# Kernel optimization log

Measured on AMD Instinct MI355X. Metric: run time of the kernel, lower is better.

## Reference

```python
import jax, jax.numpy as jnp
import numpy as np

HSIZE = 128
E = 640000


def _init_linear(key, fan_in, fan_out):
    # torch nn.Linear default init: U(-1/sqrt(fan_in), 1/sqrt(fan_in))
    kw, kb = jax.random.split(key)
    bound = 1.0 / np.sqrt(fan_in)
    W = jax.random.uniform(kw, (fan_in, fan_out), jnp.float32, -bound, bound)
    b = jax.random.uniform(kb, (fan_out,), jnp.float32, -bound, bound)
    return W, b


def setup_inputs() -> dict:
    key = jax.random.key(0)
    ks = jax.random.split(key, 6)
    hself = jax.random.normal(ks[0], (E, HSIZE), jnp.float32)
    hother = jax.random.normal(ks[1], (E, HSIZE), jnp.float32)
    Wm1, bm1 = _init_linear(ks[2], 2 * HSIZE, HSIZE)
    Wm2, bm2 = _init_linear(ks[3], HSIZE, HSIZE)
    Wu1, bu1 = _init_linear(ks[4], 2 * HSIZE, HSIZE)
    Wu2, bu2 = _init_linear(ks[5], HSIZE, HSIZE)
    return {"hself": hself, "hother": hother,
            "Wm1": Wm1, "bm1": bm1, "Wm2": Wm2, "bm2": bm2,
            "Wu1": Wu1, "bu1": bu1, "Wu2": Wu2, "bu2": bu2}


def _mlp2(a, b, W1, b1, W2, b2):
    # concat([a, b], -1) @ W1 done without materializing the concat
    h = a @ W1[:HSIZE] + b @ W1[HSIZE:] + b1
    h = jax.nn.relu(h)
    return h @ W2 + b2


def reference(hself, hother, Wm1, bm1, Wm2, bm2, Wu1, bu1, Wu2, bu2):
    # msg: Linear(2h,h) -> ReLU -> Linear(h,h) on cat([hself, hother])
    msg = _mlp2(hself, hother, Wm1, bm1, Wm2, bm2)
    # upd: Linear(2h,h) -> ReLU -> Linear(h,h) on cat([hself, msg])
    out = _mlp2(hself, msg, Wu1, bu1, Wu2, bu2)
    return out
```

## Files before the change

### kernel.cpp

```cpp
#include <hip/hip_runtime.h>

typedef __bf16 bf16_t;
typedef __bf16 bf16x8 __attribute__((ext_vector_type(8)));
typedef float f32x4 __attribute__((ext_vector_type(4)));

#define MFMA(a, b, c) __builtin_amdgcn_mfma_f32_16x16x32_bf16((a), (b), (c), 0, 0, 0)

#define E_ROWS 640000
#define BM 256
#define NTILE 2500
#define GRID 250

static __device__ __forceinline__ bf16x8 cvt8(float4 a, float4 b) {
  bf16x8 r;
  r[0] = (bf16_t)a.x; r[1] = (bf16_t)a.y; r[2] = (bf16_t)a.z; r[3] = (bf16_t)a.w;
  r[4] = (bf16_t)b.x; r[5] = (bf16_t)b.y; r[6] = (bf16_t)b.z; r[7] = (bf16_t)b.w;
  return r;
}

static __device__ __forceinline__ unsigned int pk2(float a, float b) {
  unsigned short ua = __builtin_bit_cast(unsigned short, (bf16_t)a);
  unsigned short ub = __builtin_bit_cast(unsigned short, (bf16_t)b);
  return ((unsigned int)ub << 16) | ua;
}

static __device__ __forceinline__ void gload_lds16(const void* g, void* l) {
  __builtin_amdgcn_global_load_lds(
      (const __attribute__((address_space(1))) unsigned int*)g,
      (__attribute__((address_space(3))) unsigned int*)l, 16, 0, 0);
}

__global__ __launch_bounds__(256) void prep_weights(
    const float* __restrict__ Wm1, const float* __restrict__ Wm2,
    const float* __restrict__ Wu1, const float* __restrict__ Wu2,
    bf16_t* __restrict__ wt) {
  int c = blockIdx.x * 256 + threadIdx.x;
  if (c >= 12288) return;
  int lane = c & 63, f = c >> 6;
  const float* W; int base;
  if (f < 64)       { W = Wm1; base = 0;   }
  else if (f < 96)  { W = Wm2; base = 64;  }
  else if (f < 160) { W = Wu1; base = 96;  }
  else              { W = Wu2; base = 160; }
  int fl = f - base;
  int ks = fl >> 3, nb = fl & 7;
  int k0 = 32 * ks + 8 * (lane >> 4);
  int n  = 16 * nb + (lane & 15);
  bf16x8 v;
  #pragma unroll
  for (int j = 0; j < 8; ++j) v[j] = (bf16_t)W[(size_t)(k0 + j) * 128 + n];
  ((bf16x8*)wt)[c] = v;
}

#define STAGE96(tc0) { \
  _Pragma("unroll") \
  for (int i_ = 0; i_ < 12; ++i_) \
    gload_lds16((const char*)wt + ((size_t)((tc0) + i_ * 512 + tid)) * 16, \
                smem + (i_ * 512 + tid) * 16); }

#define LDW8(s, base, fl0) \
  s##0 = *(const bf16x8*)((base) + ((fl0) + 0) * 1024 + lane * 16); \
  s##1 = *(const bf16x8*)((base) + ((fl0) + 1) * 1024 + lane * 16); \
  s##2 = *(const bf16x8*)((base) + ((fl0) + 2) * 1024 + lane * 16); \
  s##3 = *(const bf16x8*)((base) + ((fl0) + 3) * 1024 + lane * 16); \
  s##4 = *(const bf16x8*)((base) + ((fl0) + 4) * 1024 + lane * 16); \
  s##5 = *(const bf16x8*)((base) + ((fl0) + 5) * 1024 + lane * 16); \
  s##6 = *(const bf16x8*)((base) + ((fl0) + 6) * 1024 + lane * 16); \
  s##7 = *(const bf16x8*)((base) + ((fl0) + 7) * 1024 + lane * 16);

#define ROUND(s, x0, x1) \
  acc00 = MFMA(s##0, x0, acc00); acc10 = MFMA(s##0, x1, acc10); \
  acc01 = MFMA(s##1, x0, acc01); acc11 = MFMA(s##1, x1, acc11); \
  acc02 = MFMA(s##2, x0, acc02); acc12 = MFMA(s##2, x1, acc12); \
  acc03 = MFMA(s##3, x0, acc03); acc13 = MFMA(s##3, x1, acc13); \
  acc04 = MFMA(s##4, x0, acc04); acc14 = MFMA(s##4, x1, acc14); \
  acc05 = MFMA(s##5, x0, acc05); acc15 = MFMA(s##5, x1, acc15); \
  acc06 = MFMA(s##6, x0, acc06); acc16 = MFMA(s##6, x1, acc16); \
  acc07 = MFMA(s##7, x0, acc07); acc17 = MFMA(s##7, x1, acc17);

#define ACCINIT(bp) { const float* bp_ = (bp) + g * 4; float4 q; \
  q = *(const float4*)(bp_ +   0); acc00 = (f32x4){q.x,q.y,q.z,q.w}; acc10 = acc00; \
  q = *(const float4*)(bp_ +  16); acc01 = (f32x4){q.x,q.y,q.z,q.w}; acc11 = acc01; \
  q = *(const float4*)(bp_ +  32); acc02 = (f32x4){q.x,q.y,q.z,q.w}; acc12 = acc02; \
  q = *(const float4*)(bp_ +  48); acc03 = (f32x4){q.x,q.y,q.z,q.w}; acc13 = acc03; \
  q = *(const float4*)(bp_ +  64); acc04 = (f32x4){q.x,q.y,q.z,q.w}; acc14 = acc04; \
  q = *(const float4*)(bp_ +  80); acc05 = (f32x4){q.x,q.y,q.z,q.w}; acc15 = acc05; \
  q = *(const float4*)(bp_ +  96); acc06 = (f32x4){q.x,q.y,q.z,q.w}; acc16 = acc06; \
  q = *(const float4*)(bp_ + 112); acc07 = (f32x4){q.x,q.y,q.z,q.w}; acc17 = acc07; }

#define RPK_H(av, nb, R) { \
  f32x4 v = av; \
  float e0 = v[0], e1 = v[1], e2 = v[2], e3 = v[3]; \
  if (R) { e0 = fmaxf(e0, 0.f); e1 = fmaxf(e1, 0.f); \
           e2 = fmaxf(e2, 0.f); e3 = fmaxf(e3, 0.f); } \
  uint2 w; w.x = pk2(e0, e1); w.y = pk2(e2, e3); \
  int dl = c + 16 * (2 * ((nb) & 1) + (g >> 1)); \
  *(uint2*)(myrep + (((nb) >> 1) * 64 + dl) * 16 + (g & 1) * 8) = w; }

#define WAITLDS asm volatile("s_waitcnt lgkmcnt(0)" ::: "memory");
#define VMCNT0  asm volatile("s_waitcnt vmcnt(0)" ::: "memory");
#define VMCNT16 asm volatile("s_waitcnt vmcnt(16)" ::: "memory");

#define REPACK(R, x) \
  RPK_H(acc00, 0, R) RPK_H(acc01, 1, R) RPK_H(acc02, 2, R) RPK_H(acc03, 3, R) \
  RPK_H(acc04, 4, R) RPK_H(acc05, 5, R) RPK_H(acc06, 6, R) RPK_H(acc07, 7, R) \
  WAITLDS \
  x##00 = *(const bf16x8*)(myrep + (0 * 64 + lane) * 16); \
  x##01 = *(const bf16x8*)(myrep + (1 * 64 + lane) * 16); \
  x##02 = *(const bf16x8*)(myrep + (2 * 64 + lane) * 16); \
  x##03 = *(const bf16x8*)(myrep + (3 * 64 + lane) * 16); \
  WAITLDS \
  RPK_H(acc10, 0, R) RPK_H(acc11, 1, R) RPK_H(acc12, 2, R) RPK_H(acc13, 3, R) \
  RPK_H(acc14, 4, R) RPK_H(acc15, 5, R) RPK_H(acc16, 6, R) RPK_H(acc17, 7, R) \
  WAITLDS \
  x##10 = *(const bf16x8*)(myrep + (0 * 64 + lane) * 16); \
  x##11 = *(const bf16x8*)(myrep + (1 * 64 + lane) * 16); \
  x##12 = *(const bf16x8*)(myrep + (2 * 64 + lane) * 16); \
  x##13 = *(const bf16x8*)(myrep + (3 * 64 + lane) * 16); \
  WAITLDS

#define LOADX(d0, d1, basep, kk, rr0, rr1) { \
  float4 a0 = *(const float4*)((basep) + (rr0) + (kk) * 32); \
  float4 a1 = *(const float4*)((basep) + (rr0) + (kk) * 32 + 4); \
  float4 b0 = *(const float4*)((basep) + (rr1) + (kk) * 32); \
  float4 b1 = *(const float4*)((basep) + (rr1) + (kk) * 32 + 4); \
  d0 = cvt8(a0, a1); d1 = cvt8(b0, b1); }

#define LOADX4(pfx, basep, rr0, rr1) \
  LOADX(pfx##00, pfx##10, basep, 0, rr0, rr1) \
  LOADX(pfx##01, pfx##11, basep, 1, rr0, rr1) \
  LOADX(pfx##02, pfx##12, basep, 2, rr0, rr1) \
  LOADX(pfx##03, pfx##13, basep, 3, rr0, rr1)

#define ST(av, mt, nb, rb) { f32x4 v = av; \
  *(float4*)(out + ((rb) + (mt) * 16 + c) * 128 + (nb) * 16 + g * 4) = \
      (float4){v[0], v[1], v[2], v[3]}; }

#define FIRST_HALF(hs, x) \
  ACCINIT(bm1) \
  LDW8(wa, W1, 0)   ROUND(wa, hs##00, hs##10) \
  LDW8(wa, W1, 8)   ROUND(wa, hs##01, hs##11) \
  LDW8(wa, W1, 16)  ROUND(wa, hs##02, hs##12) \
  LDW8(wa, W1, 24)  ROUND(wa, hs##03, hs##13) \
  LDW8(wa, W1, 32)  ROUND(wa, x##00, x##10) \
  LDW8(wa, W1, 40)  ROUND(wa, x##01, x##11) \
  LDW8(wa, W1, 48)  ROUND(wa, x##02, x##12) \
  LDW8(wa, W1, 56)  ROUND(wa, x##03, x##13) \
  REPACK(true, x) \
  ACCINIT(bm2) \
  LDW8(wa, W2, 0)   ROUND(wa, x##00, x##10) \
  LDW8(wa, W2, 8)   ROUND(wa, x##01, x##11) \
  LDW8(wa, W2, 16)  ROUND(wa, x##02, x##12) \
  LDW8(wa, W2, 24)  ROUND(wa, x##03, x##13) \
  REPACK(false, x)

#define SECOND_HALF(hs, x, rb) \
  ACCINIT(bu1) \
  LDW8(wa, W1, 0)   ROUND(wa, hs##00, hs##10) \
  LDW8(wa, W1, 8)   ROUND(wa, hs##01, hs##11) \
  LDW8(wa, W1, 16)  ROUND(wa, hs##02, hs##12) \
  LDW8(wa, W1, 24)  ROUND(wa, hs##03, hs##13) \
  LDW8(wa, W1, 32)  ROUND(wa, x##00, x##10) \
  LDW8(wa, W1, 40)  ROUND(wa, x##01, x##11) \
  LDW8(wa, W1, 48)  ROUND(wa, x##02, x##12) \
  LDW8(wa, W1, 56)  ROUND(wa, x##03, x##13) \
  REPACK(true, x) \
  ACCINIT(bu2) \
  LDW8(wa, W2, 0)   ROUND(wa, x##00, x##10) \
  LDW8(wa, W2, 8)   ROUND(wa, x##01, x##11) \
  LDW8(wa, W2, 16)  ROUND(wa, x##02, x##12) \
  LDW8(wa, W2, 24)  ROUND(wa, x##03, x##13) \
  ST(acc00, 0, 0, rb) ST(acc01, 0, 1, rb) ST(acc02, 0, 2, rb) ST(acc03, 0, 3, rb) \
  ST(acc04, 0, 4, rb) ST(acc05, 0, 5, rb) ST(acc06, 0, 6, rb) ST(acc07, 0, 7, rb) \
  ST(acc10, 1, 0, rb) ST(acc11, 1, 1, rb) ST(acc12, 1, 2, rb) ST(acc13, 1, 3, rb) \
  ST(acc14, 1, 4, rb) ST(acc15, 1, 5, rb) ST(acc16, 1, 6, rb) ST(acc17, 1, 7, rb)

__global__ __launch_bounds__(512) void fused_mp(
    const float* __restrict__ hself, const float* __restrict__ hother,
    const bf16_t* __restrict__ wt,
    const float* __restrict__ bm1, const float* __restrict__ bm2,
    const float* __restrict__ bu1, const float* __restrict__ bu2,
    float* __restrict__ out) {
  __shared__ char smem[131072];

  const int tid = threadIdx.x;
  const int lane = tid & 63;
  const int wave = tid >> 6;
  const int c = lane & 15;
  const int g = lane >> 4;

  char* W1 = smem;
  char* W2 = smem + 65536;
  char* myrep = smem + 98304 + wave * 4096;

  bf16x8 hsA00, hsA01, hsA02, hsA03, hsA10, hsA11, hsA12, hsA13;
  bf16x8 xA00, xA01, xA02, xA03, xA10, xA11, xA12, xA13;
  bf16x8 hsB00, hsB01, hsB02, hsB03, hsB10, hsB11, hsB12, hsB13;
  bf16x8 xB00, xB01, xB02, xB03, xB10, xB11, xB12, xB13;
  f32x4 acc00, acc01, acc02, acc03, acc04, acc05, acc06, acc07;
  f32x4 acc10, acc11, acc12, acc13, acc14, acc15, acc16, acc17;
  bf16x8 wa0, wa1, wa2, wa3, wa4, wa5, wa6, wa7;

  {
    STAGE96(0)
    __builtin_amdgcn_sched_barrier(0);
    size_t rb = (size_t)blockIdx.x * BM + wave * 32;
    size_t rr0 = (rb + c) * 128 + g * 8, rr1 = rr0 + 2048;
    LOADX4(hsA, hself, rr0, rr1)
    LOADX4(xA, hother, rr0, rr1)
    VMCNT0
    __syncthreads();
  }

  #pragma unroll 1
  for (int it = 0; it < 5; ++it) {
    const int tA = blockIdx.x + it * 500;
    const int tB = tA + 250;
    int tN = tA + 500; if (tN >= NTILE) tN = 0;

    const size_t rbA = (size_t)tA * BM + wave * 32;
    const size_t rbB = (size_t)tB * BM + wave * 32;
    const size_t rbN = (size_t)tN * BM + wave * 32;
    const size_t r0B = (rbB + c) * 128 + g * 8, r1B = r0B + 2048;
    const size_t r0N = (rbN + c) * 128 + g * 8, r1N = r0N + 2048;

    FIRST_HALF(hsA, xA)
    __syncthreads();
    STAGE96(6144)
    __builtin_amdgcn_sched_barrier(0);
    LOADX4(xB, hother, r0B, r1B)
    VMCNT16
    __syncthreads();
    SECOND_HALF(hsA, xA, rbA)
    __syncthreads();
    LOADX4(hsB, hself, r0B, r1B)
    STAGE96(0)
    VMCNT0
    __syncthreads();

    FIRST_HALF(hsB, xB)
    __syncthreads();
    STAGE96(6144)
    __builtin_amdgcn_sched_barrier(0);
    LOADX4(xA, hother, r0N, r1N)
    VMCNT16
    __syncthreads();
    SECOND_HALF(hsB, xB, rbB)
    __syncthreads();
    LOADX4(hsA, hself, r0N, r1N)
    STAGE96(0)
    VMCNT0
    __syncthreads();
  }
}

extern "C" void kernel_launch(void* const* d_in, const int* in_sizes, int n_in,
                              void* d_out, int out_size, void* d_ws, size_t ws_size,
                              hipStream_t stream) {
  const float* hself  = (const float*)d_in[0];
  const float* hother = (const float*)d_in[1];
  const float* Wm1 = (const float*)d_in[2];
  const float* bm1 = (const float*)d_in[3];
  const float* Wm2 = (const float*)d_in[4];
  const float* bm2 = (const float*)d_in[5];
  const float* Wu1 = (const float*)d_in[6];
  const float* bu1 = (const float*)d_in[7];
  const float* Wu2 = (const float*)d_in[8];
  const float* bu2 = (const float*)d_in[9];
  float* out = (float*)d_out;
  bf16_t* wt = (bf16_t*)d_ws;

  prep_weights<<<48, 256, 0, stream>>>(Wm1, Wm2, Wu1, Wu2, wt);
  fused_mp<<<GRID, 512, 0, stream>>>(hself, hother, wt,
                                     bm1, bm2, bu1, bu2, out);
}
```

Baseline: 345.0 us.

## Reschedule hself loads and output stores to overlap with weight staging

Drops the double-buffered hself registers: hself for each tile is now loaded right before its first MLP instead of being prefetched. Output stores move after the weight restaging, separated by scheduling barriers, so the stores overlap with the LDS staging. The last iteration no longer prefetches a dummy tile. This frees registers and removes redundant loads, but exposes the hself load latency at the start of each tile.

After: 340.9 us. No clear change (-1.2%).

```diff
diff --git a/kernel.cpp b/kernel.cpp
--- a/kernel.cpp
+++ b/kernel.cpp
@@ -100,6 +100,7 @@
 #define WAITLDS asm volatile("s_waitcnt lgkmcnt(0)" ::: "memory");
 #define VMCNT0  asm volatile("s_waitcnt vmcnt(0)" ::: "memory");
 #define VMCNT16 asm volatile("s_waitcnt vmcnt(16)" ::: "memory");
+#define SBAR    __builtin_amdgcn_sched_barrier(0);
 
 #define REPACK(R, x) \
   RPK_H(acc00, 0, R) RPK_H(acc01, 1, R) RPK_H(acc02, 2, R) RPK_H(acc03, 3, R) \
@@ -136,12 +137,18 @@
   *(float4*)(out + ((rb) + (mt) * 16 + c) * 128 + (nb) * 16 + g * 4) = \
       (float4){v[0], v[1], v[2], v[3]}; }
 
-#define FIRST_HALF(hs, x) \
+#define STORE16(rb) \
+  ST(acc00, 0, 0, rb) ST(acc01, 0, 1, rb) ST(acc02, 0, 2, rb) ST(acc03, 0, 3, rb) \
+  ST(acc04, 0, 4, rb) ST(acc05, 0, 5, rb) ST(acc06, 0, 6, rb) ST(acc07, 0, 7, rb) \
+  ST(acc10, 1, 0, rb) ST(acc11, 1, 1, rb) ST(acc12, 1, 2, rb) ST(acc13, 1, 3, rb) \
+  ST(acc14, 1, 4, rb) ST(acc15, 1, 5, rb) ST(acc16, 1, 6, rb) ST(acc17, 1, 7, rb)
+
+#define FIRST_HALF(x) \
   ACCINIT(bm1) \
-  LDW8(wa, W1, 0)   ROUND(wa, hs##00, hs##10) \
-  LDW8(wa, W1, 8)   ROUND(wa, hs##01, hs##11) \
-  LDW8(wa, W1, 16)  ROUND(wa, hs##02, hs##12) \
-  LDW8(wa, W1, 24)  ROUND(wa, hs##03, hs##13) \
+  LDW8(wa, W1, 0)   ROUND(wa, hs00, hs10) \
+  LDW8(wa, W1, 8)   ROUND(wa, hs01, hs11) \
+  LDW8(wa, W1, 16)  ROUND(wa, hs02, hs12) \
+  LDW8(wa, W1, 24)  ROUND(wa, hs03, hs13) \
   LDW8(wa, W1, 32)  ROUND(wa, x##00, x##10) \
   LDW8(wa, W1, 40)  ROUND(wa, x##01, x##11) \
   LDW8(wa, W1, 48)  ROUND(wa, x##02, x##12) \
@@ -154,12 +161,12 @@
   LDW8(wa, W2, 24)  ROUND(wa, x##03, x##13) \
   REPACK(false, x)
 
-#define SECOND_HALF(hs, x, rb) \
+#define SECOND_HALF_NOST(x) \
   ACCINIT(bu1) \
-  LDW8(wa, W1, 0)   ROUND(wa, hs##00, hs##10) \
-  LDW8(wa, W1, 8)   ROUND(wa, hs##01, hs##11) \
-  LDW8(wa, W1, 16)  ROUND(wa, hs##02, hs##12) \
-  LDW8(wa, W1, 24)  ROUND(wa, hs##03, hs##13) \
+  LDW8(wa, W1, 0)   ROUND(wa, hs00, hs10) \
+  LDW8(wa, W1, 8)   ROUND(wa, hs01, hs11) \
+  LDW8(wa, W1, 16)  ROUND(wa, hs02, hs12) \
+  LDW8(wa, W1, 24)  ROUND(wa, hs03, hs13) \
   LDW8(wa, W1, 32)  ROUND(wa, x##00, x##10) \
   LDW8(wa, W1, 40)  ROUND(wa, x##01, x##11) \
   LDW8(wa, W1, 48)  ROUND(wa, x##02, x##12) \
@@ -169,11 +176,7 @@
   LDW8(wa, W2, 0)   ROUND(wa, x##00, x##10) \
   LDW8(wa, W2, 8)   ROUND(wa, x##01, x##11) \
   LDW8(wa, W2, 16)  ROUND(wa, x##02, x##12) \
-  LDW8(wa, W2, 24)  ROUND(wa, x##03, x##13) \
-  ST(acc00, 0, 0, rb) ST(acc01, 0, 1, rb) ST(acc02, 0, 2, rb) ST(acc03, 0, 3, rb) \
-  ST(acc04, 0, 4, rb) ST(acc05, 0, 5, rb) ST(acc06, 0, 6, rb) ST(acc07, 0, 7, rb) \
-  ST(acc10, 1, 0, rb) ST(acc11, 1, 1, rb) ST(acc12, 1, 2, rb) ST(acc13, 1, 3, rb) \
-  ST(acc14, 1, 4, rb) ST(acc15, 1, 5, rb) ST(acc16, 1, 6, rb) ST(acc17, 1, 7, rb)
+  LDW8(wa, W2, 24)  ROUND(wa, x##03, x##13)
 
 __global__ __launch_bounds__(512) void fused_mp(
     const float* __restrict__ hself, const float* __restrict__ hother,
@@ -193,9 +196,8 @@
   char* W2 = smem + 65536;
   char* myrep = smem + 98304 + wave * 4096;
 
-  bf16x8 hsA00, hsA01, hsA02, hsA03, hsA10, hsA11, hsA12, hsA13;
+  bf16x8 hs00, hs01, hs02, hs03, hs10, hs11, hs12, hs13;
   bf16x8 xA00, xA01, xA02, xA03, xA10, xA11, xA12, xA13;
-  bf16x8 hsB00, hsB01, hsB02, hsB03, hsB10, hsB11, hsB12, hsB13;
   bf16x8 xB00, xB01, xB02, xB03, xB10, xB11, xB12, xB13;
   f32x4 acc00, acc01, acc02, acc03, acc04, acc05, acc06, acc07;
   f32x4 acc10, acc11, acc12, acc13, acc14, acc15, acc16, acc17;
@@ -203,10 +205,9 @@
 
   {
     STAGE96(0)
-    __builtin_amdgcn_sched_barrier(0);
+    SBAR
     size_t rb = (size_t)blockIdx.x * BM + wave * 32;
     size_t rr0 = (rb + c) * 128 + g * 8, rr1 = rr0 + 2048;
-    LOADX4(hsA, hself, rr0, rr1)
     LOADX4(xA, hother, rr0, rr1)
     VMCNT0
     __syncthreads();
@@ -216,40 +217,52 @@
   for (int it = 0; it < 5; ++it) {
     const int tA = blockIdx.x + it * 500;
     const int tB = tA + 250;
-    int tN = tA + 500; if (tN >= NTILE) tN = 0;
 
     const size_t rbA = (size_t)tA * BM + wave * 32;
     const size_t rbB = (size_t)tB * BM + wave * 32;
-    const size_t rbN = (size_t)tN * BM + wave * 32;
+    const size_t r0A = (rbA + c) * 128 + g * 8, r1A = r0A + 2048;
     const size_t r0B = (rbB + c) * 128 + g * 8, r1B = r0B + 2048;
-    const size_t r0N = (rbN + c) * 128 + g * 8, r1N = r0N + 2048;
-
-    FIRST_HALF(hsA, xA)
+
+    LOADX4(hs, hself, r0A, r1A)
+    FIRST_HALF(xA)
     __syncthreads();
     STAGE96(6144)
-    __builtin_amdgcn_sched_barrier(0);
+    SBAR
     LOADX4(xB, hother, r0B, r1B)
+    SBAR
     VMCNT16
     __syncthreads();
-    SECOND_HALF(hsA, xA, rbA)
-    __syncthreads();
-    LOADX4(hsB, hself, r0B, r1B)
+    SECOND_HALF_NOST(xA)
+    __syncthreads();
     STAGE96(0)
-    VMCNT0
-    __syncthreads();
-
-    FIRST_HALF(hsB, xB)
+    SBAR
+    STORE16(rbA)
+    SBAR
+    VMCNT16
+    __syncthreads();
+
+    LOADX4(hs, hself, r0B, r1B)
+    FIRST_HALF(xB)
     __syncthreads();
     STAGE96(6144)
-    __builtin_amdgcn_sched_barrier(0);
-    LOADX4(xA, hother, r0N, r1N)
+    SBAR
+    if (it < 4) {
+      const size_t rbN = (size_t)(tA + 500) * BM + wave * 32;
+      const size_t r0N = (rbN + c) * 128 + g * 8, r1N = r0N + 2048;
+      LOADX4(xA, hother, r0N, r1N)
+      SBAR
+      VMCNT16
+    } else {
+      VMCNT0
+    }
+    __syncthreads();
+    SECOND_HALF_NOST(xB)
+    __syncthreads();
+    STAGE96(0)
+    SBAR
+    STORE16(rbB)
+    SBAR
     VMCNT16
-    __syncthreads();
-    SECOND_HALF(hsB, xB, rbB)
-    __syncthreads();
-    LOADX4(hsA, hself, r0N, r1N)
-    STAGE96(0)
-    VMCNT0
     __syncthreads();
   }
 }
```
